# Kernel optimization log

Hardware: AMD Instinct MI355X
Metric: run time of the kernel (lower is better)

## Reference

```python
import jax, jax.numpy as jnp
import numpy as np

BITS = 4
SIGNED_MIN, SIGNED_MAX = -(2 ** (BITS - 1)), 2 ** (BITS - 1) - 1      # int4: [-8, 7]
UNSIGNED_MIN, UNSIGNED_MAX = 0, 2 ** BITS - 1                          # uint4: [0, 15]
INT32_MIN, INT32_MAX = -(2.0 ** 31), 2.0 ** 31 - 1


def fake_quant(x, scale, qmin, qmax):
    """Brevitas-style fake quantization with straight-through rounding."""
    q = jnp.clip(jnp.round(x / scale), qmin, qmax) * scale
    # STE: identity gradient through round/clip
    return x + jax.lax.stop_gradient(q - x)


def weight_scale(W):
    # Brevitas default weight quantizer: per-tensor scale from max-abs stats
    return jax.lax.stop_gradient(jnp.max(jnp.abs(W))) / SIGNED_MAX


def setup_inputs() -> dict:
    key = jax.random.key(0)
    ks = jax.random.split(key, 5)
    B, S, D, F = 4, 2048, 2048, 8192
    return {
        "x": jax.random.normal(ks[0], (B, S, D), dtype=jnp.float32),
        "W1": jax.random.normal(ks[1], (F, D), dtype=jnp.float32) * 0.02,
        "b1": jax.random.normal(ks[2], (F,), dtype=jnp.float32) * 0.02,
        "W2": jax.random.normal(ks[3], (D, F), dtype=jnp.float32) * 0.02,
        "b2": jax.random.normal(ks[4], (D,), dtype=jnp.float32) * 0.02,
        "s_act1": jnp.full((1,), 0.1, dtype=jnp.float32),
        "s_act2": jnp.full((1,), 0.1, dtype=jnp.float32),
    }


def reference(x, W1, b1, W2, b2, s_act1, s_act2):
    s1 = s_act1[0]
    s2 = s_act2[0]

    # quantizer_1: signed int4 QuantIdentity on input
    x_q = fake_quant(x, s1, SIGNED_MIN, SIGNED_MAX)

    # w_1: int4 weight QuantLinear with Int32Bias (bias scale = in_scale * w_scale)
    sw1 = weight_scale(W1)
    W1_q = fake_quant(W1, sw1, SIGNED_MIN, SIGNED_MAX)
    b1_q = fake_quant(b1, s1 * sw1, INT32_MIN, INT32_MAX)
    h = jnp.einsum("bsd,fd->bsf", x_q, W1_q) + b1_q  # [B, S, d_ff]

    # quantizer_2: QuantReLU -> unsigned int4 fake-quant of relu(h)
    h_q = fake_quant(jax.nn.relu(h), s2, UNSIGNED_MIN, UNSIGNED_MAX)
    # dropout: identity in eval mode

    # w_2: int4 weight QuantLinear, input scale = s2
    sw2 = weight_scale(W2)
    W2_q = fake_quant(W2, sw2, SIGNED_MIN, SIGNED_MAX)
    b2_q = fake_quant(b2, s2 * sw2, INT32_MIN, INT32_MAX)
    out = jnp.einsum("bsf,df->bsd", h_q, W2_q) + b2_q  # [B, S, d_model]
    return out
```

## Files before the change

kernel.cpp:

```cpp
#include <hip/hip_runtime.h>

typedef int int32x4 __attribute__((ext_vector_type(4)));


__global__ void prep_kernel(const float* __restrict__ W1,
                            const float* __restrict__ W2,
                            const float* __restrict__ x, int n4,
                            int Kx, int kshiftx,
                            const float* __restrict__ s1,
                            unsigned* __restrict__ mx, int* __restrict__ xq) {
    int i0 = blockIdx.x * blockDim.x + threadIdx.x;
    int stride = gridDim.x * blockDim.x;
    if (blockIdx.y < 2) {
        const float4* x4 = (const float4*)(blockIdx.y ? W2 : W1);
        float m = 0.f;
        for (int j = i0; j < n4; j += stride) {
            float4 v = x4[j];
            m = fmaxf(m, fmaxf(fmaxf(fabsf(v.x), fabsf(v.y)),
                               fmaxf(fabsf(v.z), fabsf(v.w))));
        }
#pragma unroll
        for (int off = 32; off; off >>= 1)
            m = fmaxf(m, __shfl_down(m, off, 64));
        __shared__ float wm[4];
        int ln = threadIdx.x & 63, wv = threadIdx.x >> 6;
        if (ln == 0) wm[wv] = m;
        __syncthreads();
        if (threadIdx.x == 0) {
            float bm = fmaxf(fmaxf(wm[0], wm[1]), fmaxf(wm[2], wm[3]));
            atomicMax(mx + blockIdx.y, __float_as_uint(bm));
        }
    } else {
        float s = s1[0];
        for (int o = i0; o < n4; o += stride) {
            int blk = o >> 12;
            int i = o & 4095;
            int row = i >> 5;
            int c = (i >> 2) & 7;
            int b4 = i & 3;
            int rowblk = blk >> kshiftx;
            int kblk = blk & ((1 << kshiftx) - 1);
            int co = c ^ (row & 7);
            long srcoff = (long)(rowblk * 128 + row) * Kx + (kblk << 7) + (co << 4) + (b4 << 2);
            float4 f = *(const float4*)(x + srcoff);
            int a = (int)fminf(fmaxf(rintf(f.x / s), -8.f), 7.f);
            int b = (int)fminf(fmaxf(rintf(f.y / s), -8.f), 7.f);
            int cc = (int)fminf(fmaxf(rintf(f.z / s), -8.f), 7.f);
            int d = (int)fminf(fmaxf(rintf(f.w / s), -8.f), 7.f);
            xq[o] = (a & 255) | ((b & 255) << 8) | ((cc & 255) << 16) | ((d & 255) << 24);
        }
    }
}

__global__ void quantW_kernel(const float* __restrict__ W1,
                              const float* __restrict__ W2, int n4,
                              int K1, int ks1, int K2, int ks2,
                              const unsigned* __restrict__ mx,
                              int* __restrict__ w1q, int* __restrict__ w2q) {
    const int y = blockIdx.y;
    const float* src = y ? W2 : W1;
    int* out = y ? w2q : w1q;
    const int K = y ? K2 : K1;
    const int kshift = y ? ks2 : ks1;
    float s = __uint_as_float(mx[y]) / 7.0f;
    int i0 = blockIdx.x * blockDim.x + threadIdx.x;
    int stride = gridDim.x * blockDim.x;
    for (int o = i0; o < n4; o += stride) {
        int blk = o >> 12;
        int i = o & 4095;
        int row = i >> 5;
        int c = (i >> 2) & 7;
        int b4 = i & 3;
        int rowblk = blk >> kshift;
        int kblk = blk & ((1 << kshift) - 1);
        int co = c ^ (row & 7);
        long srcoff = (long)(rowblk * 128 + row) * K + (kblk << 7) + (co << 4) + (b4 << 2);
        float4 f = *(const float4*)(src + srcoff);
        int a = (int)fminf(fmaxf(rintf(f.x / s), -8.f), 7.f);
        int b = (int)fminf(fmaxf(rintf(f.y / s), -8.f), 7.f);
        int cc = (int)fminf(fmaxf(rintf(f.z / s), -8.f), 7.f);
        int d = (int)fminf(fmaxf(rintf(f.w / s), -8.f), 7.f);
        out[o] = (a & 255) | ((b & 255) << 8) | ((cc & 255) << 16) | ((d & 255) << 24);
    }
}

template <bool FIRST>
__global__ __launch_bounds__(256, 2)
void gemm_i8_kernel(const char* __restrict__ A, const char* __restrict__ B,
                    int N, int nkt,
                    const float* __restrict__ sa_ptr,
                    const float* __restrict__ wmax_ptr,
                    const float* __restrict__ bias,
                    const float* __restrict__ s2_ptr,
                    char* __restrict__ out8, float* __restrict__ outf) {
    __shared__ __align__(16) char lA[128 * 128];
    __shared__ __align__(16) char lB[128 * 128];

    const int tid = threadIdx.x;
    const int wv = tid >> 6, ln = tid & 63;
    const int lnlo = ln & 15, lnhi = ln >> 4;
    const int wr = wv >> 1, wc = wv & 1;

    int32x4 acc[4][4] = {};

    const char* pa = A + ((size_t)blockIdx.y * nkt << 14);
    const char* pb = B + ((size_t)blockIdx.x * nkt << 14);

    for (int kt = 0; kt < nkt; ++kt) {
#pragma unroll
        for (int r = 0; r < 4; ++r) {
            int off = (r * 256 + tid) * 16;
            int lbase = (r * 256 + wv * 64) * 16;
            __builtin_amdgcn_global_load_lds(
                (const __attribute__((address_space(1))) void*)(pa + off),
                (__attribute__((address_space(3))) void*)(lA + lbase), 16, 0, 0);
            __builtin_amdgcn_global_load_lds(
                (const __attribute__((address_space(1))) void*)(pb + off),
                (__attribute__((address_space(3))) void*)(lB + lbase), 16, 0, 0);
        }
        pa += 16384;
        pb += 16384;
        __syncthreads();

        int32x4 af[4][2], bf[4][2];
#pragma unroll
        for (int mf = 0; mf < 4; ++mf)
#pragma unroll
            for (int kk = 0; kk < 2; ++kk) {
                int row = wr * 64 + mf * 16 + lnlo;
                int ch = kk * 4 + lnhi;
                af[mf][kk] = *(const int32x4*)(lA + row * 128 + ((ch ^ (row & 7)) * 16));
            }
#pragma unroll
        for (int nf = 0; nf < 4; ++nf)
#pragma unroll
            for (int kk = 0; kk < 2; ++kk) {
                int col = wc * 64 + nf * 16 + lnlo;
                int ch = kk * 4 + lnhi;
                bf[nf][kk] = *(const int32x4*)(lB + col * 128 + ((ch ^ (col & 7)) * 16));
            }

#pragma unroll
        for (int kk = 0; kk < 2; ++kk)
#pragma unroll
            for (int mf = 0; mf < 4; ++mf)
#pragma unroll
                for (int nf = 0; nf < 4; ++nf)
                    acc[mf][nf] = __builtin_amdgcn_mfma_i32_16x16x64_i8(
                        af[mf][kk], bf[nf][kk], acc[mf][nf], 0, 0, 0);
        __syncthreads();
    }

    float sa = sa_ptr[0];
    float sw = wmax_ptr[0] / 7.0f;
    float sab = sa * sw;
    float s2v = FIRST ? s2_ptr[0] : 0.f;

    char* hblk = FIRST ? out8 + (((size_t)blockIdx.y * gridDim.x + blockIdx.x) << 14)
                       : nullptr;

#pragma unroll
    for (int nf = 0; nf < 4; ++nf) {
        int lc = wc * 64 + nf * 16 + lnlo;
        long col = (long)blockIdx.x * 128 + lc;
        float bq = rintf(bias[col] / sab) * sab;
#pragma unroll
        for (int mf = 0; mf < 4; ++mf) {
            int lr0 = wr * 64 + mf * 16 + (lnhi << 2);
#pragma unroll
            for (int i = 0; i < 4; ++i) {
                int lr = lr0 + i;
                float h = sab * (float)acc[mf][nf][i] + bq;
                if constexpr (FIRST) {
                    h = fmaxf(h, 0.f);
                    float qv = fminf(fmaxf(rintf(h / s2v), 0.f), 15.f);
                    hblk[lr * 128 + (((lc >> 4) ^ (lr & 7)) << 4) + (lc & 15)] =
                        (char)(int)qv;
                } else {
                    outf[((long)blockIdx.y * 128 + lr) * N + col] = h;
                }
            }
        }
    }
}

extern "C" void kernel_launch(void* const* d_in, const int* in_sizes, int n_in,
                              void* d_out, int out_size, void* d_ws, size_t ws_size,
                              hipStream_t stream) {
    const float* x  = (const float*)d_in[0];
    const float* W1 = (const float*)d_in[1];
    const float* b1 = (const float*)d_in[2];
    const float* W2 = (const float*)d_in[3];
    const float* b2 = (const float*)d_in[4];
    const float* s1 = (const float*)d_in[5];
    const float* s2 = (const float*)d_in[6];

    const int M = 8192, D = 2048, F = 8192;

    char* ws = (char*)d_ws;
    unsigned* mx = (unsigned*)ws;
    char* xq  = ws + 256;
    char* w1q = xq + (size_t)M * D;
    char* w2q = w1q + (size_t)F * D;
    char* hq  = w2q + (size_t)D * F;

    hipMemsetAsync(d_ws, 0, 8, stream);

    const int n4 = (F * D) >> 2;
    prep_kernel<<<dim3(2048, 3), 256, 0, stream>>>(
        W1, W2, x, n4, D, 4, s1, mx, (int*)xq);

    quantW_kernel<<<dim3(2048, 2), 256, 0, stream>>>(
        W1, W2, n4, D, 4, F, 6, mx, (int*)w1q, (int*)w2q);

    gemm_i8_kernel<true><<<dim3(F / 128, M / 128), 256, 0, stream>>>(
        xq, w1q, F, D / 128, s1, (const float*)mx, b1, s2, hq, nullptr);

    gemm_i8_kernel<false><<<dim3(D / 128, M / 128), 256, 0, stream>>>(
        hq, w2q, D, F / 128, s2, (const float*)(mx + 1), b2, nullptr, nullptr,
        (float*)d_out);
}
```

Before: 363.7 us.

## Switch int8 GEMMs to scaled fp8 MFMA with exact fp8-encoded int4 values

```diff
diff --git a/kernel.cpp b/kernel.cpp
--- a/kernel.cpp
+++ b/kernel.cpp
@@ -1,6 +1,16 @@
 #include <hip/hip_runtime.h>
 
 typedef int int32x4 __attribute__((ext_vector_type(4)));
+typedef int int32x8 __attribute__((ext_vector_type(8)));
+typedef float floatx4 __attribute__((ext_vector_type(4)));
+
+__device__ __forceinline__ unsigned fp8e(int n) {
+    const unsigned long long tA = 0x4E4C4A4844403800ULL;
+    const unsigned long long tB = 0x5756555453525150ULL;
+    int m = n < 0 ? -n : n;
+    unsigned b = (unsigned)(((m < 8) ? (tA >> (8 * m)) : (tB >> (8 * (m - 8)))) & 0xFF);
+    return b | ((unsigned)(n < 0) << 7);
+}
 
 
 __global__ void prep_kernel(const float* __restrict__ W1,
@@ -47,7 +57,7 @@
             int b = (int)fminf(fmaxf(rintf(f.y / s), -8.f), 7.f);
             int cc = (int)fminf(fmaxf(rintf(f.z / s), -8.f), 7.f);
             int d = (int)fminf(fmaxf(rintf(f.w / s), -8.f), 7.f);
-            xq[o] = (a & 255) | ((b & 255) << 8) | ((cc & 255) << 16) | ((d & 255) << 24);
+            xq[o] = fp8e(a) | (fp8e(b) << 8) | (fp8e(cc) << 16) | (fp8e(d) << 24);
         }
     }
 }
@@ -80,19 +90,19 @@
         int b = (int)fminf(fmaxf(rintf(f.y / s), -8.f), 7.f);
         int cc = (int)fminf(fmaxf(rintf(f.z / s), -8.f), 7.f);
         int d = (int)fminf(fmaxf(rintf(f.w / s), -8.f), 7.f);
-        out[o] = (a & 255) | ((b & 255) << 8) | ((cc & 255) << 16) | ((d & 255) << 24);
+        out[o] = fp8e(a) | (fp8e(b) << 8) | (fp8e(cc) << 16) | (fp8e(d) << 24);
     }
 }
 
 template <bool FIRST>
 __global__ __launch_bounds__(256, 2)
-void gemm_i8_kernel(const char* __restrict__ A, const char* __restrict__ B,
-                    int N, int nkt,
-                    const float* __restrict__ sa_ptr,
-                    const float* __restrict__ wmax_ptr,
-                    const float* __restrict__ bias,
-                    const float* __restrict__ s2_ptr,
-                    char* __restrict__ out8, float* __restrict__ outf) {
+void gemm_fp8_kernel(const char* __restrict__ A, const char* __restrict__ B,
+                     int N, int nkt,
+                     const float* __restrict__ sa_ptr,
+                     const float* __restrict__ wmax_ptr,
+                     const float* __restrict__ bias,
+                     const float* __restrict__ s2_ptr,
+                     char* __restrict__ out8, float* __restrict__ outf) {
     __shared__ __align__(16) char lA[128 * 128];
     __shared__ __align__(16) char lB[128 * 128];
 
@@ -101,7 +111,7 @@
     const int lnlo = ln & 15, lnhi = ln >> 4;
     const int wr = wv >> 1, wc = wv & 1;
 
-    int32x4 acc[4][4] = {};
+    floatx4 acc[4][4] = {};
 
     const char* pa = A + ((size_t)blockIdx.y * nkt << 14);
     const char* pb = B + ((size_t)blockIdx.x * nkt << 14);
@@ -122,32 +132,33 @@
         pb += 16384;
         __syncthreads();
 
-        int32x4 af[4][2], bf[4][2];
+        int32x8 af[4], bf[4];
+#pragma unroll
+        for (int mf = 0; mf < 4; ++mf) {
+            int row = wr * 64 + mf * 16 + lnlo;
+            int c0 = (2 * lnhi) ^ (row & 7);
+            int c1 = (2 * lnhi + 1) ^ (row & 7);
+            int32x4 p = *(const int32x4*)(lA + row * 128 + c0 * 16);
+            int32x4 q = *(const int32x4*)(lA + row * 128 + c1 * 16);
+            af[mf] = __builtin_shufflevector(p, q, 0, 1, 2, 3, 4, 5, 6, 7);
+        }
+#pragma unroll
+        for (int nf = 0; nf < 4; ++nf) {
+            int col = wc * 64 + nf * 16 + lnlo;
+            int c0 = (2 * lnhi) ^ (col & 7);
+            int c1 = (2 * lnhi + 1) ^ (col & 7);
+            int32x4 p = *(const int32x4*)(lB + col * 128 + c0 * 16);
+            int32x4 q = *(const int32x4*)(lB + col * 128 + c1 * 16);
+            bf[nf] = __builtin_shufflevector(p, q, 0, 1, 2, 3, 4, 5, 6, 7);
+        }
+
 #pragma unroll
         for (int mf = 0; mf < 4; ++mf)
 #pragma unroll
-            for (int kk = 0; kk < 2; ++kk) {
-                int row = wr * 64 + mf * 16 + lnlo;
-                int ch = kk * 4 + lnhi;
-                af[mf][kk] = *(const int32x4*)(lA + row * 128 + ((ch ^ (row & 7)) * 16));
-            }
-#pragma unroll
-        for (int nf = 0; nf < 4; ++nf)
-#pragma unroll
-            for (int kk = 0; kk < 2; ++kk) {
-                int col = wc * 64 + nf * 16 + lnlo;
-                int ch = kk * 4 + lnhi;
-                bf[nf][kk] = *(const int32x4*)(lB + col * 128 + ((ch ^ (col & 7)) * 16));
-            }
-
-#pragma unroll
-        for (int kk = 0; kk < 2; ++kk)
-#pragma unroll
-            for (int mf = 0; mf < 4; ++mf)
-#pragma unroll
-                for (int nf = 0; nf < 4; ++nf)
-                    acc[mf][nf] = __builtin_amdgcn_mfma_i32_16x16x64_i8(
-                        af[mf][kk], bf[nf][kk], acc[mf][nf], 0, 0, 0);
+            for (int nf = 0; nf < 4; ++nf)
+                acc[mf][nf] = __builtin_amdgcn_mfma_scale_f32_16x16x128_f8f6f4(
+                    af[mf], bf[nf], acc[mf][nf], 0, 0,
+                    0, 0x7F7F7F7F, 0, 0x7F7F7F7F);
         __syncthreads();
     }
 
@@ -170,12 +181,12 @@
 #pragma unroll
             for (int i = 0; i < 4; ++i) {
                 int lr = lr0 + i;
-                float h = sab * (float)acc[mf][nf][i] + bq;
+                float h = sab * acc[mf][nf][i] + bq;
                 if constexpr (FIRST) {
                     h = fmaxf(h, 0.f);
-                    float qv = fminf(fmaxf(rintf(h / s2v), 0.f), 15.f);
+                    int qv = (int)fminf(fmaxf(rintf(h / s2v), 0.f), 15.f);
                     hblk[lr * 128 + (((lc >> 4) ^ (lr & 7)) << 4) + (lc & 15)] =
-                        (char)(int)qv;
+                        (char)fp8e(qv);
                 } else {
                     outf[((long)blockIdx.y * 128 + lr) * N + col] = h;
                 }
@@ -213,10 +224,10 @@
     quantW_kernel<<<dim3(2048, 2), 256, 0, stream>>>(
         W1, W2, n4, D, 4, F, 6, mx, (int*)w1q, (int*)w2q);
 
-    gemm_i8_kernel<true><<<dim3(F / 128, M / 128), 256, 0, stream>>>(
+    gemm_fp8_kernel<true><<<dim3(F / 128, M / 128), 256, 0, stream>>>(
         xq, w1q, F, D / 128, s1, (const float*)mx, b1, s2, hq, nullptr);
 
-    gemm_i8_kernel<false><<<dim3(D / 128, M / 128), 256, 0, stream>>>(
+    gemm_fp8_kernel<false><<<dim3(D / 128, M / 128), 256, 0, stream>>>(
         hq, w2q, D, F / 128, s2, (const float*)(mx + 1), b2, nullptr, nullptr,
         (float*)d_out);
 }
```

Result: slower. 380.7 us (+4.7%).
